# Kernel optimization log

Measured on AMD Instinct MI355X. Metric: run time of the kernel, lower is better.

## Reference

```python
import jax, jax.numpy as jnp
import numpy as np

B, D, U = 4096, 1024, 1024

def cumax(a):
    # Faithful to source: softmax over last axis, cumsum over axis 0 (TF defaults).
    return jnp.cumsum(jax.nn.softmax(a, axis=-1), axis=0)

def setup_inputs() -> dict:
    key = jax.random.key(0)
    ks = jax.random.split(key, 21)
    names = ['inputs', 'hidden_prev', 'cell_prev',
             'Wf', 'Uf', 'bf', 'Wi', 'Ui', 'bi', 'Wo', 'Uo', 'bo',
             'Wc', 'Uc', 'bc', 'Wft', 'Uft', 'bft', 'Wit', 'Uit', 'bit']
    shapes = [(B, D), (B, U), (B, U)] + [(D, U), (U, U), (U,)] * 6
    scales = [1.0, 1.0, 1.0] + [0.05, 0.05, 0.05] * 6  # random_normal init ~ small stddev
    return {n: jax.random.normal(k, s, dtype=jnp.float32) * sc
            for n, k, s, sc in zip(names, ks, shapes, scales)}

def reference(inputs, hidden_prev, cell_prev,
              Wf, Uf, bf, Wi, Ui, bi, Wo, Uo, bo,
              Wc, Uc, bc, Wft, Uft, bft, Wit, Uit, bit):
    # Fuse the 12 small GEMMs into 2 big ones: [B,D]@[D,6U] and [B,U]@[U,6U]
    W_all = jnp.concatenate([Wf, Wi, Wo, Wc, Wft, Wit], axis=1)   # [D, 6U]
    U_all = jnp.concatenate([Uf, Ui, Uo, Uc, Uft, Uit], axis=1)   # [U, 6U]
    b_all = jnp.concatenate([bf, bi, bo, bc, bft, bit], axis=0)   # [6U]
    pre = inputs @ W_all + hidden_prev @ U_all + b_all            # [B, 6U]
    zf, zi, zo, zc, zft, zit = [pre[:, j*U:(j+1)*U] for j in range(6)]

    f = jax.nn.sigmoid(zf)
    i = jax.nn.sigmoid(zi)
    o = jax.nn.sigmoid(zo)
    c_hat = jnp.tanh(zc)
    f_tilde = cumax(zft)
    i_tilde = 1.0 - cumax(zit)

    omega = f_tilde * i_tilde
    f_hat = f * omega + (f_tilde - omega)
    i_hat = i * omega + (i_tilde - omega)
    cell = f_hat * cell_prev + i_hat * c_hat
    hidden = o * jnp.tanh(cell)
    return hidden, cell
```

## Files before the change

kernel.cpp:

```cpp
#include <hip/hip_runtime.h>
#include <cstdint>
#include <cstddef>


typedef _Float16 half8  __attribute__((ext_vector_type(8)));
typedef _Float16 half4v __attribute__((ext_vector_type(4)));
typedef float f32x4 __attribute__((ext_vector_type(4)));

__device__ __forceinline__ void async16(const _Float16* g, _Float16* l) {
  __builtin_amdgcn_global_load_lds(
      (const __attribute__((address_space(1))) void*)g,
      (__attribute__((address_space(3))) void*)l, 16, 0, 0);
}

struct Ptrs12 { const float* p[12]; };
struct Ptrs6  { const float* p[6];  };

__global__ void prep(const float* __restrict__ X, const float* __restrict__ H,
                     Ptrs12 w, Ptrs6 bs,
                     _Float16* __restrict__ Ahi, _Float16* __restrict__ Bhi,
                     float* __restrict__ b_all) {
  __shared__ float tile[64][65];
  const int blk = blockIdx.x;
  const int t = threadIdx.x;
  if (blk < 8192) {
    size_t base = ((size_t)blk * 256 + t) * 4;
    int k = (int)(base & 2047);
    size_t b = base >> 11;
    const float* src = (k < 1024) ? (X + b * 1024 + k) : (H + b * 1024 + (k - 1024));
    float4 v = *(const float4*)src;
    half4v hi = { (_Float16)v.x, (_Float16)v.y, (_Float16)v.z, (_Float16)v.w };
    *(half4v*)(Ahi + base) = hi;
  } else if (blk < 11264) {
    int bb = blk - 8192;
    int mat = bb >> 8;
    int tl = bb & 255;
    int tr = tl >> 4, tc = tl & 15;
    int g = mat >> 1, s = mat & 1;
    const float* src = w.p[mat];
    int col = t & 63, r0 = t >> 6;
#pragma unroll
    for (int i = 0; i < 16; i++) {
      int row = i * 4 + r0;
      tile[row][col] = src[(size_t)(tr * 64 + row) * 1024 + tc * 64 + col];
    }
    __syncthreads();
    int c2 = t >> 2, kseg = t & 3;
    half8 v0, v1;
#pragma unroll
    for (int j = 0; j < 8; j++) {
      v0[j] = (_Float16)(tile[kseg * 16 + j][c2] * 64.0f);
      v1[j] = (_Float16)(tile[kseg * 16 + 8 + j][c2] * 64.0f);
    }
    size_t n  = (size_t)g * 1024 + tc * 64 + c2;
    size_t kk = (size_t)s * 1024 + tr * 64 + kseg * 16;
    *(half8*)(Bhi + n * 2048 + kk) = v0;
    *(half8*)(Bhi + n * 2048 + kk + 8) = v1;
  } else {
    int n = (blk - 11264) * 256 + t;
    b_all[n] = bs.p[n >> 10][n & 1023];
  }
}


#define LGKM0 asm volatile("s_waitcnt lgkmcnt(0)" ::: "memory")

__device__ __forceinline__ void wg_barrier() {
  __builtin_amdgcn_s_barrier();
  asm volatile("" ::: "memory");
}

__global__ __launch_bounds__(512, 2) void gemm_ring(
    const _Float16* __restrict__ Ah, const _Float16* __restrict__ Bh,
    const float* __restrict__ b_all, _Float16* __restrict__ pre16) {
  __shared__ __attribute__((aligned(16))) _Float16 lds[73728];

  const int bid = blockIdx.x;
  const int swz = (bid & 7) * 96 + (bid >> 3);
  const int nTile = swz / 32;
  const int mTile = swz % 32;

  const int t = threadIdx.x;
  const int lane = t & 63;
  const int wave = t >> 6;
  const int wm = wave >> 2, wn = wave & 3;
  const int kgrp = lane >> 4, frow = lane & 15;

  const _Float16* Abase = Ah + (size_t)mTile * 128 * 2048;
  const _Float16* Bbase = Bh + (size_t)nTile * 256 * 2048;

  f32x4 acc[4][4] = {};

  auto stage_tile = [&](int kt, int base) {
#pragma unroll
    for (int q = 0; q < 2; q++) {
      int s = q * 512 + t;
      int r = s >> 3, k8 = s & 7;
      int xs = k8 ^ (r & 7);
      async16(Abase + (size_t)r * 2048 + kt * 64 + xs * 8, lds + base + s * 8);
    }
#pragma unroll
    for (int q = 0; q < 4; q++) {
      int s = q * 512 + t;
      int r = s >> 3, k8 = s & 7;
      int xs = k8 ^ (r & 7);
      async16(Bbase + (size_t)r * 2048 + kt * 64 + xs * 8,
              lds + base + 8192 + s * 8);
    }
  };

  int cur = 0, nxt = 24576, nn = 49152;

  stage_tile(0, cur);
  stage_tile(1, nxt);
  asm volatile("s_waitcnt vmcnt(6)" ::: "memory");
  wg_barrier();

  for (int T = 0; T < 32; T++) {
    const _Float16* A_ = lds + cur;
    const _Float16* B_ = lds + cur + 8192;
    half8 af[4][2], bf[4][2];
#pragma unroll
    for (int mi = 0; mi < 4; mi++) {
      int r = wm * 64 + mi * 16 + frow;
#pragma unroll
      for (int ks = 0; ks < 2; ks++)
        af[mi][ks] = *(const half8*)(A_ + r * 64 +
                                     (((ks * 4 + kgrp) ^ (r & 7)) * 8));
    }
#pragma unroll
    for (int nj = 0; nj < 4; nj++) {
      int r = wn * 64 + nj * 16 + frow;
#pragma unroll
      for (int ks = 0; ks < 2; ks++)
        bf[nj][ks] = *(const half8*)(B_ + r * 64 +
                                     (((ks * 4 + kgrp) ^ (r & 7)) * 8));
    }
    if (T + 2 < 32) stage_tile(T + 2, nn);

    __builtin_amdgcn_s_setprio(1);
#pragma unroll
    for (int mi = 0; mi < 4; mi++)
#pragma unroll
      for (int nj = 0; nj < 4; nj++)
        acc[mi][nj] = __builtin_amdgcn_mfma_f32_16x16x32_f16(
            af[mi][0], bf[nj][0], acc[mi][nj], 0, 0, 0);
    __builtin_amdgcn_s_setprio(0);

    LGKM0;
    if (T < 30) {
      asm volatile("s_waitcnt vmcnt(6)" ::: "memory");
      wg_barrier();
    } else if (T == 30) {
      asm volatile("s_waitcnt vmcnt(0)" ::: "memory");
      wg_barrier();
    }

    __builtin_amdgcn_s_setprio(1);
#pragma unroll
    for (int mi = 0; mi < 4; mi++)
#pragma unroll
      for (int nj = 0; nj < 4; nj++)
        acc[mi][nj] = __builtin_amdgcn_mfma_f32_16x16x32_f16(
            af[mi][1], bf[nj][1], acc[mi][nj], 0, 0, 0);
    __builtin_amdgcn_s_setprio(0);

    int tmp = cur; cur = nxt; nxt = nn; nn = tmp;
  }

  __syncthreads();
  const float inv64 = 1.0f / 64.0f;
  const int cb = nTile * 256;
  float bias[4];
#pragma unroll
  for (int nj = 0; nj < 4; nj++)
    bias[nj] = b_all[cb + wn * 64 + nj * 16 + frow];
#pragma unroll
  for (int mi = 0; mi < 4; mi++) {
#pragma unroll
    for (int nj = 0; nj < 4; nj++) {
      int row = wm * 64 + mi * 16 + kgrp * 4;
      int col = wn * 64 + nj * 16 + frow;
#pragma unroll
      for (int j = 0; j < 4; j++)
        lds[(row + j) * 264 + col] =
            (_Float16)(acc[mi][nj][j] * inv64 + bias[nj]);
    }
  }
  __syncthreads();
#pragma unroll
  for (int rr = 0; rr < 8; rr++) {
    int L = rr * 4096 + t * 8;
    int row = L >> 8, col = L & 255;
    half8 v = *(const half8*)(lds + row * 264 + col);
    *(half8*)(pre16 + (size_t)(mTile * 128 + row) * 6144 + cb + col) = v;
  }
}

__global__ void softmax_partials(_Float16* __restrict__ pre16, f32x4* __restrict__ part4) {
  __shared__ float wsum[4][1024];
  int m = blockIdx.x >> 9;
  int ch = blockIdx.x & 511;
  int t = threadIdx.x;
  int wave = t >> 6, lane = t & 63;
  f32x4 colacc[4] = {};
  for (int rr = 0; rr < 2; rr++) {
    int b = ch * 8 + wave * 2 + rr;
    _Float16* row = pre16 + (size_t)b * 6144 + (4 + m) * 1024;
    f32x4 v[4];
    float mx = -3.4e38f;
#pragma unroll
    for (int j = 0; j < 4; j++) {
      half4v h = *(const half4v*)(row + lane * 4 + 256 * j);
      v[j] = f32x4{ (float)h[0], (float)h[1], (float)h[2], (float)h[3] };
      mx = fmaxf(mx, fmaxf(fmaxf(v[j][0], v[j][1]), fmaxf(v[j][2], v[j][3])));
    }
#pragma unroll
    for (int off = 32; off > 0; off >>= 1) mx = fmaxf(mx, __shfl_xor(mx, off, 64));
    float sum = 0.f;
#pragma unroll
    for (int j = 0; j < 4; j++)
#pragma unroll
      for (int q = 0; q < 4; q++) { v[j][q] = __expf(v[j][q] - mx); sum += v[j][q]; }
#pragma unroll
    for (int off = 32; off > 0; off >>= 1) sum += __shfl_xor(sum, off, 64);
    float inv = 1.f / sum;
#pragma unroll
    for (int j = 0; j < 4; j++) {
      v[j] *= inv;
      half4v h = { (_Float16)v[j][0], (_Float16)v[j][1], (_Float16)v[j][2], (_Float16)v[j][3] };
      *(half4v*)(row + lane * 4 + 256 * j) = h;
      colacc[j] += v[j];
    }
  }
#pragma unroll
  for (int j = 0; j < 4; j++)
    *(f32x4*)(&wsum[wave][lane * 4 + 256 * j]) = colacc[j];
  __syncthreads();
  f32x4 s = *(const f32x4*)(&wsum[0][t * 4]);
  s += *(const f32x4*)(&wsum[1][t * 4]);
  s += *(const f32x4*)(&wsum[2][t * 4]);
  s += *(const f32x4*)(&wsum[3][t * 4]);
  part4[((size_t)m * 256 + t) * 512 + ch] = s;
}

__global__ void scan_partials(const f32x4* __restrict__ part4, f32x4* __restrict__ off4) {
  int gidx = blockIdx.x * 4 + (threadIdx.x >> 6);
  int lane = threadIdx.x & 63;
  size_t base = (size_t)gidx * 512;
  f32x4 v[8];
  f32x4 s = {};
#pragma unroll
  for (int j = 0; j < 8; j++) {
    v[j] = part4[base + lane * 8 + j];
    s += v[j];
  }
  f32x4 incl = s;
#pragma unroll
  for (int off = 1; off < 64; off <<= 1) {
    f32x4 o;
#pragma unroll
    for (int q = 0; q < 4; q++) o[q] = __shfl_up(incl[q], off, 64);
    if (lane >= off) incl += o;
  }
  f32x4 run = incl - s;
#pragma unroll
  for (int j = 0; j < 8; j++) {
    off4[base + lane * 8 + j] = run;
    run += v[j];
  }
}

__global__ void onlstm_final(const _Float16* __restrict__ pre16,
                             const float* __restrict__ cprev, const f32x4* __restrict__ off4,
                             float* __restrict__ out) {
  int ch = blockIdx.x;
  int c4 = threadIdx.x;
  int c = c4 * 4;
  f32x4 runf = off4[(size_t)c4 * 512 + ch];
  f32x4 runi = off4[(size_t)(256 + c4) * 512 + ch];
  for (int r = 0; r < 8; r++) {
    int b = ch * 8 + r;
    const _Float16* row = pre16 + (size_t)b * 6144;
    half4v zf = *(const half4v*)(row + c);
    half4v zi = *(const half4v*)(row + 1024 + c);
    half4v zo = *(const half4v*)(row + 2048 + c);
    half4v zc = *(const half4v*)(row + 3072 + c);
    half4v pf = *(const half4v*)(row + 4096 + c);
    half4v pi = *(const half4v*)(row + 5120 + c);
    f32x4 cp = *(const f32x4*)(cprev + (size_t)b * 1024 + c);
    f32x4 hid, cel;
#pragma unroll
    for (int q = 0; q < 4; q++) {
      runf[q] += (float)pf[q];
      runi[q] += (float)pi[q];
      float ft = runf[q], it = 1.f - runi[q];
      float f  = 1.f / (1.f + __expf(-(float)zf[q]));
      float ii = 1.f / (1.f + __expf(-(float)zi[q]));
      float o  = 1.f / (1.f + __expf(-(float)zo[q]));
      float chat = tanhf((float)zc[q]);
      float omega = ft * it;
      float fhat = f * omega + (ft - omega);
      float ihat = ii * omega + (it - omega);
      float cell = fhat * cp[q] + ihat * chat;
      hid[q] = o * tanhf(cell);
      cel[q] = cell;
    }
    *(f32x4*)(out + (size_t)b * 1024 + c) = hid;
    *(f32x4*)(out + (size_t)4194304 + (size_t)b * 1024 + c) = cel;
  }
}

extern "C" void kernel_launch(void* const* d_in, const int* in_sizes, int n_in,
                              void* d_out, int out_size, void* d_ws, size_t ws_size,
                              hipStream_t stream) {
  const float* X = (const float*)d_in[0];
  const float* H = (const float*)d_in[1];
  const float* C = (const float*)d_in[2];

  char* ws = (char*)d_ws;
  _Float16* pre16 = (_Float16*)(ws);
  _Float16* Ahi   = (_Float16*)(ws + 50331648);
  _Float16* Bhi   = (_Float16*)(ws + 67108864);
  float*    b_all = (float*)(ws + 92274688);
  f32x4*    part4 = (f32x4*)(ws + 92299264);
  f32x4*    off4  = (f32x4*)(ws + 96493568);

  Ptrs12 w;
  for (int g = 0; g < 6; g++) {
    w.p[2 * g]     = (const float*)d_in[3 + 3 * g];
    w.p[2 * g + 1] = (const float*)d_in[4 + 3 * g];
  }
  Ptrs6 bs;
  for (int g = 0; g < 6; g++) bs.p[g] = (const float*)d_in[5 + 3 * g];

  prep<<<11288, 256, 0, stream>>>(X, H, w, bs, Ahi, Bhi, b_all);
  gemm_ring<<<768, 512, 0, stream>>>(Ahi, Bhi, b_all, pre16);
  softmax_partials<<<1024, 256, 0, stream>>>(pre16, part4);
  scan_partials<<<128, 256, 0, stream>>>(part4, off4);
  onlstm_final<<<512, 256, 0, stream>>>(pre16, C, off4, (float*)d_out);
}
```

Measured before the change: 314.4 us.

## Halve GEMM K-tile to 32 and raise occupancy to four workgroups per CU

The fp16 MFMA GEMM now uses a K-step of 32 instead of 64, shrinking the triple-buffered LDS ring from 144KB to 72KB. Launch bounds move from 2 to 4 workgroups per CU. The XOR swizzle is adapted to 4 slots per row, and the single barrier per iteration now sits before the MFMAs, replacing the old split mid-iteration wait. The goal is more resident waves to hide latency, at the cost of twice as many barriers and LDS round trips per unit of K, plus tighter register limits.

```diff
diff --git a/kernel.cpp b/kernel.cpp
--- a/kernel.cpp
+++ b/kernel.cpp
@@ -70,10 +70,10 @@
   asm volatile("" ::: "memory");
 }
 
-__global__ __launch_bounds__(512, 2) void gemm_ring(
+__global__ __launch_bounds__(512, 4) void gemm_ring32(
     const _Float16* __restrict__ Ah, const _Float16* __restrict__ Bh,
     const float* __restrict__ b_all, _Float16* __restrict__ pre16) {
-  __shared__ __attribute__((aligned(16))) _Float16 lds[73728];
+  __shared__ __attribute__((aligned(16))) _Float16 lds[36864];
 
   const int bid = blockIdx.x;
   const int swz = (bid & 7) * 96 + (bid >> 3);
@@ -92,51 +92,52 @@
   f32x4 acc[4][4] = {};
 
   auto stage_tile = [&](int kt, int base) {
+    {
+      int r = t >> 2, sl = t & 3;
+      int xs = sl ^ (r & 3);
+      async16(Abase + (size_t)r * 2048 + kt * 32 + xs * 8, lds + base + t * 8);
+    }
 #pragma unroll
     for (int q = 0; q < 2; q++) {
       int s = q * 512 + t;
-      int r = s >> 3, k8 = s & 7;
-      int xs = k8 ^ (r & 7);
-      async16(Abase + (size_t)r * 2048 + kt * 64 + xs * 8, lds + base + s * 8);
-    }
-#pragma unroll
-    for (int q = 0; q < 4; q++) {
-      int s = q * 512 + t;
-      int r = s >> 3, k8 = s & 7;
-      int xs = k8 ^ (r & 7);
-      async16(Bbase + (size_t)r * 2048 + kt * 64 + xs * 8,
-              lds + base + 8192 + s * 8);
+      int r = s >> 2, sl = s & 3;
+      int xs = sl ^ (r & 3);
+      async16(Bbase + (size_t)r * 2048 + kt * 32 + xs * 8,
+              lds + base + 4096 + s * 8);
     }
   };
 
-  int cur = 0, nxt = 24576, nn = 49152;
+  int cur = 0, nxt = 12288, nn = 24576;
 
   stage_tile(0, cur);
   stage_tile(1, nxt);
-  asm volatile("s_waitcnt vmcnt(6)" ::: "memory");
+  asm volatile("s_waitcnt vmcnt(3)" ::: "memory");
   wg_barrier();
 
-  for (int T = 0; T < 32; T++) {
+  for (int T = 0; T < 64; T++) {
     const _Float16* A_ = lds + cur;
-    const _Float16* B_ = lds + cur + 8192;
-    half8 af[4][2], bf[4][2];
+    const _Float16* B_ = lds + cur + 4096;
+    half8 af[4], bf[4];
 #pragma unroll
     for (int mi = 0; mi < 4; mi++) {
       int r = wm * 64 + mi * 16 + frow;
-#pragma unroll
-      for (int ks = 0; ks < 2; ks++)
-        af[mi][ks] = *(const half8*)(A_ + r * 64 +
-                                     (((ks * 4 + kgrp) ^ (r & 7)) * 8));
+      af[mi] = *(const half8*)(A_ + r * 32 + ((kgrp ^ (r & 3)) * 8));
     }
 #pragma unroll
     for (int nj = 0; nj < 4; nj++) {
       int r = wn * 64 + nj * 16 + frow;
-#pragma unroll
-      for (int ks = 0; ks < 2; ks++)
-        bf[nj][ks] = *(const half8*)(B_ + r * 64 +
-                                     (((ks * 4 + kgrp) ^ (r & 7)) * 8));
-    }
-    if (T + 2 < 32) stage_tile(T + 2, nn);
+      bf[nj] = *(const half8*)(B_ + r * 32 + ((kgrp ^ (r & 3)) * 8));
+    }
+    if (T + 2 < 64) stage_tile(T + 2, nn);
+
+    LGKM0;
+    if (T < 62) {
+      asm volatile("s_waitcnt vmcnt(3)" ::: "memory");
+      wg_barrier();
+    } else if (T == 62) {
+      asm volatile("s_waitcnt vmcnt(0)" ::: "memory");
+      wg_barrier();
+    }
 
     __builtin_amdgcn_s_setprio(1);
 #pragma unroll
@@ -144,25 +145,7 @@
 #pragma unroll
       for (int nj = 0; nj < 4; nj++)
         acc[mi][nj] = __builtin_amdgcn_mfma_f32_16x16x32_f16(
-            af[mi][0], bf[nj][0], acc[mi][nj], 0, 0, 0);
-    __builtin_amdgcn_s_setprio(0);
-
-    LGKM0;
-    if (T < 30) {
-      asm volatile("s_waitcnt vmcnt(6)" ::: "memory");
-      wg_barrier();
-    } else if (T == 30) {
-      asm volatile("s_waitcnt vmcnt(0)" ::: "memory");
-      wg_barrier();
-    }
-
-    __builtin_amdgcn_s_setprio(1);
-#pragma unroll
-    for (int mi = 0; mi < 4; mi++)
-#pragma unroll
-      for (int nj = 0; nj < 4; nj++)
-        acc[mi][nj] = __builtin_amdgcn_mfma_f32_16x16x32_f16(
-            af[mi][1], bf[nj][1], acc[mi][nj], 0, 0, 0);
+            af[mi], bf[nj], acc[mi][nj], 0, 0, 0);
     __builtin_amdgcn_s_setprio(0);
 
     int tmp = cur; cur = nxt; nxt = nn; nn = tmp;
@@ -335,7 +318,7 @@
   for (int g = 0; g < 6; g++) bs.p[g] = (const float*)d_in[5 + 3 * g];
 
   prep<<<11288, 256, 0, stream>>>(X, H, w, bs, Ahi, Bhi, b_all);
-  gemm_ring<<<768, 512, 0, stream>>>(Ahi, Bhi, b_all, pre16);
+  gemm_ring32<<<768, 512, 0, stream>>>(Ahi, Bhi, b_all, pre16);
   softmax_partials<<<1024, 256, 0, stream>>>(pre16, part4);
   scan_partials<<<128, 256, 0, stream>>>(part4, off4);
   onlstm_final<<<512, 256, 0, stream>>>(pre16, C, off4, (float*)d_out);
```

Result: no change. 315.2 us (+0.3%).
